# Performance work log

Hardware: AMD Instinct MI355X
Metric: run time of the kernel (lower is better)

Reference implementation:

```python
import jax, jax.numpy as jnp
import numpy as np

N_NODES = 100000
N_EDGES = 3200000
IN_CH, HID, OUT_CH = 11, 64, 1


def setup_inputs() -> dict:
    key = jax.random.key(0)
    ks = jax.random.split(key, 10)
    x = jax.random.normal(ks[0], (N_NODES, IN_CH), dtype=jnp.float32)
    edge_index = jax.random.randint(ks[1], (2, N_EDGES), 0, N_NODES, dtype=jnp.int64)
    s = lambda k, shape, fan_in: jax.random.normal(k, shape, jnp.float32) * (1.0 / np.sqrt(fan_in))
    return {
        "x": x,
        "edge_index": edge_index,
        # conv1: lin_l acts on aggregated neighbors (has bias), lin_r on root (no bias)
        "Wl1": s(ks[2], (HID, IN_CH), IN_CH), "bl1": jnp.zeros((HID,), jnp.float32),
        "Wr1": s(ks[3], (HID, IN_CH), IN_CH),
        "Wl2": s(ks[4], (HID, HID), HID), "bl2": jnp.zeros((HID,), jnp.float32),
        "Wr2": s(ks[5], (HID, HID), HID),
        "Wlin": s(ks[6], (OUT_CH, HID), HID), "blin": jnp.zeros((OUT_CH,), jnp.float32),
    }


def _sage_conv(x, src, dst, Wl, bl, Wr):
    # mean aggregation of source features onto destination nodes
    msg = x[src]                                            # [E, d] gather
    agg = jax.ops.segment_sum(msg, dst, num_segments=N_NODES)          # [N, d]
    cnt = jax.ops.segment_sum(jnp.ones_like(dst, jnp.float32), dst, num_segments=N_NODES)
    mean = agg / jnp.maximum(cnt, 1.0)[:, None]             # isolated nodes -> 0
    return mean @ Wl.T + bl + x @ Wr.T


def reference(x, edge_index, Wl1, bl1, Wr1, Wl2, bl2, Wr2, Wlin, blin):
    src, dst = edge_index[0], edge_index[1]
    h = jax.nn.relu(_sage_conv(x, src, dst, Wl1, bl1, Wr1))
    h = jax.nn.relu(_sage_conv(h, src, dst, Wl2, bl2, Wr2))
    return h @ Wlin.T + blin
```

## Files before the change

### kernel.cpp

```cpp
#include <hip/hip_runtime.h>
#include <hip/hip_fp16.h>

#define IN_CH 11
#define HID 64
#define PAD 64
#define OVCAP 16384
#define NBLK 1024
#define BSH 7

typedef _Float16 half8_t __attribute__((ext_vector_type(8)));
typedef float f32x4_t __attribute__((ext_vector_type(4)));

__global__ void k_prep(const float* __restrict__ x, const float* __restrict__ Wl2,
                       const float* __restrict__ Wr2, unsigned* __restrict__ xphu,
                       __half* __restrict__ wl2h, __half* __restrict__ wr2h,
                       int* __restrict__ ovcnt, int N) {
    int i = blockIdx.x * blockDim.x + threadIdx.x;
    if (i == 0) *ovcnt = 0;
    if (i < HID * HID) {
        wl2h[i] = __float2half_rn(Wl2[i]);
        wr2h[i] = __float2half_rn(Wr2[i]);
    }
    if (i < (N + 1) * 8) {
        int n = i >> 3, j = (i & 7) * 2;
        float a = 0.f, b = 0.f;
        if (n < N) {
            if (j < IN_CH) a = x[n * IN_CH + j];
            if (j + 1 < IN_CH) b = x[n * IN_CH + j + 1];
        }
        unsigned lo = (unsigned)__half_as_ushort(__float2half_rn(a));
        unsigned hi = (unsigned)__half_as_ushort(__float2half_rn(b));
        xphu[i] = lo | (hi << 16);
    }
}


__global__ __launch_bounds__(256) void k_hist(const int* __restrict__ dst,
        int* __restrict__ hist, int E, int csz, int nbkt) {
    __shared__ int h[800];
    int tid = threadIdx.x, blk = blockIdx.x;
    for (int t = tid; t < nbkt; t += 256) h[t] = 0;
    __syncthreads();
    int c0 = blk * csz, c1 = min(c0 + csz, E);
    for (int e = c0 + tid; e < c1; e += 256)
        atomicAdd(&h[dst[e] >> BSH], 1);
    __syncthreads();
    for (int t = tid; t < nbkt; t += 256) hist[t * NBLK + blk] = h[t];
}

__global__ __launch_bounds__(1024) void k_scanA(int* __restrict__ hist,
        int* __restrict__ btot) {
    __shared__ int wsum[16];
    int b = blockIdx.x, tid = threadIdx.x;
    int lane = tid & 63, wv = tid >> 6;
    int v = hist[b * NBLK + tid];
    int inc = v;
    #pragma unroll
    for (int off = 1; off < 64; off <<= 1) {
        int t = __shfl_up(inc, off);
        if (lane >= off) inc += t;
    }
    if (lane == 63) wsum[wv] = inc;
    __syncthreads();
    int base = 0;
    #pragma unroll
    for (int w = 0; w < 16; w++) base += (w < wv) ? wsum[w] : 0;
    hist[b * NBLK + tid] = base + inc - v;
    if (tid == NBLK - 1) btot[b] = base + inc;
}

__global__ __launch_bounds__(1024) void k_scanB(const int* __restrict__ btot,
        int* __restrict__ bstart, int nbkt) {
    __shared__ int wsum[16];
    int tid = threadIdx.x;
    int lane = tid & 63, wv = tid >> 6;
    int v = (tid < nbkt) ? btot[tid] : 0;
    int inc = v;
    #pragma unroll
    for (int off = 1; off < 64; off <<= 1) {
        int t = __shfl_up(inc, off);
        if (lane >= off) inc += t;
    }
    if (lane == 63) wsum[wv] = inc;
    __syncthreads();
    int base = 0;
    #pragma unroll
    for (int w = 0; w < 16; w++) base += (w < wv) ? wsum[w] : 0;
    if (tid < nbkt) bstart[tid] = base + inc - v;
}

__global__ __launch_bounds__(256) void k_scatter(const int* __restrict__ src,
        const int* __restrict__ dst, const int* __restrict__ hist,
        const int* __restrict__ bstart,
        unsigned* __restrict__ ebuf, int E, int csz, int nbkt) {
    __shared__ int cur[800];
    int tid = threadIdx.x, blk = blockIdx.x;
    for (int t = tid; t < nbkt; t += 256)
        cur[t] = hist[t * NBLK + blk] + bstart[t];
    __syncthreads();
    int c0 = blk * csz, c1 = min(c0 + csz, E);
    for (int e = c0 + tid; e < c1; e += 256) {
        int d = dst[e], s = src[e];
        int slot = atomicAdd(&cur[d >> BSH], 1);
        ebuf[slot] = ((unsigned)(d & 127) << 17) | (unsigned)s;
    }
}

__global__ __launch_bounds__(256) void k_bbuild(const unsigned* __restrict__ ebuf,
        const int* __restrict__ bstart, const int* __restrict__ btot,
        int* __restrict__ cnt, int* __restrict__ col64,
        int* __restrict__ ovcnt, int* __restrict__ ov, int N) {
    __shared__ int lc[128];
    __shared__ int colsh[128 * PAD];
    int tid = threadIdx.x, b = blockIdx.x;
    int lo = b << BSH, hi = min(lo + 128, N);
    #pragma unroll
    for (int i = 0; i < 8; i++)
        ((int4*)colsh)[tid + i * 256] = make_int4(N, N, N, N);
    if (tid < 128) lc[tid] = 0;
    __syncthreads();
    int cs = bstart[b], cc = btot[b];
    for (int i = tid; i < cc; i += 256) {
        unsigned v = ebuf[cs + i];
        int dl = (int)(v >> 17), s = (int)(v & 0x1FFFFu);
        int r = atomicAdd(&lc[dl], 1);
        if (r < PAD) {
            colsh[(dl << 6) | r] = s;
        } else {
            int q = atomicAdd(ovcnt, 1);
            if (q < OVCAP) { ov[2 * q] = lo + dl; ov[2 * q + 1] = s; }
        }
    }
    __syncthreads();
    int nn = hi - lo;
    int4* dst4 = (int4*)col64 + (size_t)lo * 16;
    for (int i = tid; i < nn * 16; i += 256) dst4[i] = ((int4*)colsh)[i];
    if (tid < nn) cnt[lo + tid] = lc[tid];
}

__global__ void k_agg1(const unsigned* __restrict__ xphu,
                       const int* __restrict__ col64,
                       float* __restrict__ agg1, int N) {
    int lane = threadIdx.x & 63;
    int n = blockIdx.x * 4 + (threadIdx.x >> 6);
    if (n >= N) return;
    int c8 = lane & 7, sub = lane >> 3;
    const int* cb = col64 + n * PAD;
    int s[8];
    #pragma unroll
    for (int jj = 0; jj < 8; jj++) s[jj] = cb[sub + 8 * jj];
    unsigned v[8];
    #pragma unroll
    for (int jj = 0; jj < 8; jj++) v[jj] = xphu[s[jj] * 8 + c8];
    __half2 a2 = __floats2half2_rn(0.f, 0.f);
    #pragma unroll
    for (int jj = 0; jj < 8; jj++) a2 = __hadd2(a2, *(__half2*)&v[jj]);
    float2 f = __half22float2(a2);
    #pragma unroll
    for (int off = 8; off <= 32; off <<= 1) {
        f.x += __shfl_xor(f.x, off);
        f.y += __shfl_xor(f.y, off);
    }
    if (lane < 8) ((float2*)agg1)[n * 8 + lane] = f;
}

__global__ void k_ov1(const int* __restrict__ ovcnt, const int* __restrict__ ov,
                      const float* __restrict__ x, float* __restrict__ agg1) {
    int c = *ovcnt; if (c > OVCAP) c = OVCAP;
    for (int i = blockIdx.x * blockDim.x + threadIdx.x; i < c;
         i += gridDim.x * blockDim.x) {
        int d = ov[2 * i], s = ov[2 * i + 1];
        for (int ch = 0; ch < IN_CH; ch++)
            atomicAdd(&agg1[d * 16 + ch], x[s * IN_CH + ch]);
    }
}

__global__ void k_dense1(const float* __restrict__ x, const float* __restrict__ agg1,
                         const int* __restrict__ cnt, const float* __restrict__ Wl,
                         const float* __restrict__ bl, const float* __restrict__ Wr,
                         unsigned* __restrict__ h1h, int N) {
    int lane = threadIdx.x & 63;
    int n = blockIdx.x * 4 + (threadIdx.x >> 6);
    if (n > N) return;
    if (n == N) {
        if (lane < 32) h1h[n * 32 + lane] = 0u;
        return;
    }
    int deg = cnt[n];
    float inv = deg > 0 ? 1.f / (float)deg : 0.f;
    float mv = (lane < 16) ? agg1[n * 16 + lane] * inv : 0.f;
    float xv = (lane < IN_CH) ? x[n * IN_CH + lane] : 0.f;
    float h = bl[lane];
    #pragma unroll
    for (int c = 0; c < IN_CH; c++)
        h += Wl[lane * IN_CH + c] * __shfl(mv, c) + Wr[lane * IN_CH + c] * __shfl(xv, c);
    h = fmaxf(h, 0.f);
    unsigned my = (unsigned)__half_as_ushort(__float2half_rn(h));
    unsigned nx = __shfl_down(my, 1);
    if ((lane & 1) == 0) h1h[n * 32 + (lane >> 1)] = my | (nx << 16);
}

__global__ void k_agg2(const uint4* __restrict__ h1h4, const int* __restrict__ col64,
                       float* __restrict__ agg2, int N) {
    int lane = threadIdx.x & 63;
    int n = blockIdx.x * 4 + (threadIdx.x >> 6);
    if (n >= N) return;
    int c8 = lane & 7, sub = lane >> 3;
    const int* cb = col64 + n * PAD;
    int s[8];
    #pragma unroll
    for (int jj = 0; jj < 8; jj++) s[jj] = cb[sub + 8 * jj];
    uint4 v[8];
    #pragma unroll
    for (int jj = 0; jj < 8; jj++) v[jj] = h1h4[s[jj] * 8 + c8];
    __half2 a2[4];
    #pragma unroll
    for (int t = 0; t < 4; t++) a2[t] = __floats2half2_rn(0.f, 0.f);
    #pragma unroll
    for (int jj = 0; jj < 8; jj++) {
        a2[0] = __hadd2(a2[0], *(__half2*)&v[jj].x);
        a2[1] = __hadd2(a2[1], *(__half2*)&v[jj].y);
        a2[2] = __hadd2(a2[2], *(__half2*)&v[jj].z);
        a2[3] = __hadd2(a2[3], *(__half2*)&v[jj].w);
    }
    float acc[8];
    #pragma unroll
    for (int t = 0; t < 4; t++) {
        float2 f = __half22float2(a2[t]);
        acc[2 * t] = f.x; acc[2 * t + 1] = f.y;
    }
    #pragma unroll
    for (int off = 8; off <= 32; off <<= 1) {
        #pragma unroll
        for (int t = 0; t < 8; t++) acc[t] += __shfl_xor(acc[t], off);
    }
    float val = acc[0];
    #pragma unroll
    for (int t = 1; t < 8; t++) if (sub == t) val = acc[t];
    agg2[n * 64 + 8 * c8 + sub] = val;
}

__global__ void k_ov2(const int* __restrict__ ovcnt, const int* __restrict__ ov,
                      const unsigned* __restrict__ h1h, float* __restrict__ agg2) {
    int c = *ovcnt; if (c > OVCAP) c = OVCAP;
    const __half* h1 = (const __half*)h1h;
    for (int i = blockIdx.x * blockDim.x + threadIdx.x; i < c;
         i += gridDim.x * blockDim.x) {
        int d = ov[2 * i], s = ov[2 * i + 1];
        for (int ch = 0; ch < HID; ch++)
            atomicAdd(&agg2[d * 64 + ch], __half2float(h1[s * 64 + ch]));
    }
}

__global__ __launch_bounds__(256) void k_dense2(
    const float4* __restrict__ agg2_4, const int* __restrict__ cnt,
    const uint4* __restrict__ h1h_u4,
    const __half* __restrict__ wl2h, const __half* __restrict__ wr2h,
    const float* __restrict__ bl, const float* __restrict__ Wlin,
    const float* __restrict__ blin, float* __restrict__ out, int N) {
    union U { uint4 u; half8_t h; };
    int lane = threadIdx.x & 63;
    int wave = blockIdx.x * 4 + (threadIdx.x >> 6);
    int nwaves = gridDim.x * 4;
    int r16 = lane & 15, quad = lane >> 4;
    const uint4* wlu = (const uint4*)wl2h;
    const uint4* wru = (const uint4*)wr2h;
    half8_t bfr[4][4];
    #pragma unroll
    for (int tt = 0; tt < 4; tt++) {
        int o = tt * 16 + r16;
        U t0, t1, t2, t3;
        t0.u = wlu[o * 8 + quad];
        t1.u = wlu[o * 8 + 4 + quad];
        t2.u = wru[o * 8 + quad];
        t3.u = wru[o * 8 + 4 + quad];
        bfr[tt][0] = t0.h; bfr[tt][1] = t1.h; bfr[tt][2] = t2.h; bfr[tt][3] = t3.h;
    }
    float bl_c[4], wl_c[4];
    #pragma unroll
    for (int tt = 0; tt < 4; tt++) {
        bl_c[tt] = bl[tt * 16 + r16];
        wl_c[tt] = Wlin[tt * 16 + r16];
    }
    float b0 = blin[0];
    int ntiles = (N + 15) >> 4;
    for (int t = wave; t < ntiles; t += nwaves) {
        int nb = t * 16;
        int n = nb + r16; if (n >= N) n = N - 1;
        int deg = cnt[n];
        float inv = deg > 0 ? 1.f / (float)deg : 0.f;
        float4 m0 = agg2_4[n * 16 + quad * 2];
        float4 m1 = agg2_4[n * 16 + quad * 2 + 1];
        float4 m2 = agg2_4[n * 16 + 8 + quad * 2];
        float4 m3 = agg2_4[n * 16 + 8 + quad * 2 + 1];
        half8_t a0h, a1h;
        a0h[0] = (_Float16)(m0.x * inv); a0h[1] = (_Float16)(m0.y * inv);
        a0h[2] = (_Float16)(m0.z * inv); a0h[3] = (_Float16)(m0.w * inv);
        a0h[4] = (_Float16)(m1.x * inv); a0h[5] = (_Float16)(m1.y * inv);
        a0h[6] = (_Float16)(m1.z * inv); a0h[7] = (_Float16)(m1.w * inv);
        a1h[0] = (_Float16)(m2.x * inv); a1h[1] = (_Float16)(m2.y * inv);
        a1h[2] = (_Float16)(m2.z * inv); a1h[3] = (_Float16)(m2.w * inv);
        a1h[4] = (_Float16)(m3.x * inv); a1h[5] = (_Float16)(m3.y * inv);
        a1h[6] = (_Float16)(m3.z * inv); a1h[7] = (_Float16)(m3.w * inv);
        U a2, a3;
        a2.u = h1h_u4[n * 8 + quad];
        a3.u = h1h_u4[n * 8 + 4 + quad];
        float p0 = 0.f, p1 = 0.f, p2 = 0.f, p3 = 0.f;
        #pragma unroll
        for (int tt = 0; tt < 4; tt++) {
            f32x4_t c = {0.f, 0.f, 0.f, 0.f};
            c = __builtin_amdgcn_mfma_f32_16x16x32_f16(a0h, bfr[tt][0], c, 0, 0, 0);
            c = __builtin_amdgcn_mfma_f32_16x16x32_f16(a1h, bfr[tt][1], c, 0, 0, 0);
            c = __builtin_amdgcn_mfma_f32_16x16x32_f16(a2.h, bfr[tt][2], c, 0, 0, 0);
            c = __builtin_amdgcn_mfma_f32_16x16x32_f16(a3.h, bfr[tt][3], c, 0, 0, 0);
            p0 += fmaxf(c[0] + bl_c[tt], 0.f) * wl_c[tt];
            p1 += fmaxf(c[1] + bl_c[tt], 0.f) * wl_c[tt];
            p2 += fmaxf(c[2] + bl_c[tt], 0.f) * wl_c[tt];
            p3 += fmaxf(c[3] + bl_c[tt], 0.f) * wl_c[tt];
        }
        #pragma unroll
        for (int off = 1; off <= 8; off <<= 1) {
            p0 += __shfl_xor(p0, off); p1 += __shfl_xor(p1, off);
            p2 += __shfl_xor(p2, off); p3 += __shfl_xor(p3, off);
        }
        if (r16 == 0) {
            int nn = nb + quad * 4;
            if (nn + 3 < N) {
                ((float4*)out)[nn >> 2] = make_float4(p0 + b0, p1 + b0, p2 + b0, p3 + b0);
            } else {
                if (nn + 0 < N) out[nn + 0] = p0 + b0;
                if (nn + 1 < N) out[nn + 1] = p1 + b0;
                if (nn + 2 < N) out[nn + 2] = p2 + b0;
                if (nn + 3 < N) out[nn + 3] = p3 + b0;
            }
        }
    }
}


extern "C" void kernel_launch(void* const* d_in, const int* in_sizes, int n_in,
                              void* d_out, int out_size, void* d_ws, size_t ws_size,
                              hipStream_t stream) {
    const float* x    = (const float*)d_in[0];
    const int*   ei   = (const int*)d_in[1];
    const float* Wl1  = (const float*)d_in[2];
    const float* bl1  = (const float*)d_in[3];
    const float* Wr1  = (const float*)d_in[4];
    const float* Wl2  = (const float*)d_in[5];
    const float* bl2  = (const float*)d_in[6];
    const float* Wr2  = (const float*)d_in[7];
    const float* Wlin = (const float*)d_in[8];
    const float* blin = (const float*)d_in[9];
    float* out = (float*)d_out;

    int N = in_sizes[0] / IN_CH;
    int E = in_sizes[1] / 2;
    const int* srcp = ei;
    const int* dstp = ei + E;

    int* ws       = (int*)d_ws;
    int* cnt      = ws;
    int* ovcnt    = ws + N;
    int* col64    = ws + 100032;
    int* hist     = ws + 100032;
    unsigned* xph = (unsigned*)(ws + 6500032);
    unsigned* ebuf = (unsigned*)(ws + 7300064);
    float* agg1   = (float*)(ws + 7300064);
    float* agg2   = (float*)(ws + 6500032);
    unsigned* h1h = (unsigned*)(ws + 12900096);
    int* ov       = ws + 16100128;
    __half* wl2h  = (__half*)(ws + 16132896);
    __half* wr2h  = (__half*)(ws + 16134944);
    int* btot     = ws + 16136992;
    int* bstart   = ws + 16138016;

    int nbkt = (N + 127) >> BSH;
    int csz  = (E + NBLK - 1) / NBLK;

    k_prep   <<<((N + 1) * 8 + 255) / 256, 256, 0, stream>>>(x, Wl2, Wr2, xph,
                                                             wl2h, wr2h, ovcnt, N);
    k_hist   <<<NBLK, 256, 0, stream>>>(dstp, hist, E, csz, nbkt);
    k_scanA  <<<nbkt, 1024, 0, stream>>>(hist, btot);
    k_scanB  <<<1, 1024, 0, stream>>>(btot, bstart, nbkt);
    k_scatter<<<NBLK, 256, 0, stream>>>(srcp, dstp, hist, bstart, ebuf, E, csz, nbkt);
    k_bbuild <<<nbkt, 256, 0, stream>>>(ebuf, bstart, btot, cnt, col64,
                                        ovcnt, ov, N);

    k_agg1   <<<(N + 3) / 4, 256, 0, stream>>>(xph, col64, agg1, N);
    k_ov1    <<<8, 256, 0, stream>>>(ovcnt, ov, x, agg1);
    k_dense1 <<<(N + 4) / 4, 256, 0, stream>>>(x, agg1, cnt, Wl1, bl1, Wr1, h1h, N);

    k_agg2   <<<(N + 3) / 4, 256, 0, stream>>>((const uint4*)h1h, col64, agg2, N);
    k_ov2    <<<8, 256, 0, stream>>>(ovcnt, ov, h1h, agg2);

    k_dense2 <<<512, 256, 0, stream>>>((const float4*)agg2, cnt, (const uint4*)h1h,
                                       wl2h, wr2h, bl2, Wlin, blin, out, N);
}
```

Measured before the change: 293.2 us.

## Coarsen edge bucketing to 1024-node buckets with 8 sub-block builds each

```diff
diff --git a/kernel.cpp b/kernel.cpp
--- a/kernel.cpp
+++ b/kernel.cpp
@@ -5,8 +5,8 @@
 #define HID 64
 #define PAD 64
 #define OVCAP 16384
-#define NBLK 1024
-#define BSH 7
+#define NBLK 512
+#define BSH 10
 
 typedef _Float16 half8_t __attribute__((ext_vector_type(8)));
 typedef float f32x4_t __attribute__((ext_vector_type(4)));
@@ -37,20 +37,20 @@
 
 __global__ __launch_bounds__(256) void k_hist(const int* __restrict__ dst,
         int* __restrict__ hist, int E, int csz, int nbkt) {
-    __shared__ int h[800];
+    __shared__ int h[128];
     int tid = threadIdx.x, blk = blockIdx.x;
-    for (int t = tid; t < nbkt; t += 256) h[t] = 0;
+    if (tid < 128) h[tid] = 0;
     __syncthreads();
     int c0 = blk * csz, c1 = min(c0 + csz, E);
     for (int e = c0 + tid; e < c1; e += 256)
         atomicAdd(&h[dst[e] >> BSH], 1);
     __syncthreads();
-    for (int t = tid; t < nbkt; t += 256) hist[t * NBLK + blk] = h[t];
-}
-
-__global__ __launch_bounds__(1024) void k_scanA(int* __restrict__ hist,
+    if (tid < nbkt) hist[tid * NBLK + blk] = h[tid];
+}
+
+__global__ __launch_bounds__(512) void k_scanA(int* __restrict__ hist,
         int* __restrict__ btot) {
-    __shared__ int wsum[16];
+    __shared__ int wsum[8];
     int b = blockIdx.x, tid = threadIdx.x;
     int lane = tid & 63, wv = tid >> 6;
     int v = hist[b * NBLK + tid];
@@ -64,14 +64,14 @@
     __syncthreads();
     int base = 0;
     #pragma unroll
-    for (int w = 0; w < 16; w++) base += (w < wv) ? wsum[w] : 0;
+    for (int w = 0; w < 8; w++) base += (w < wv) ? wsum[w] : 0;
     hist[b * NBLK + tid] = base + inc - v;
     if (tid == NBLK - 1) btot[b] = base + inc;
 }
 
-__global__ __launch_bounds__(1024) void k_scanB(const int* __restrict__ btot,
+__global__ __launch_bounds__(128) void k_scanB(const int* __restrict__ btot,
         int* __restrict__ bstart, int nbkt) {
-    __shared__ int wsum[16];
+    __shared__ int wsum[2];
     int tid = threadIdx.x;
     int lane = tid & 63, wv = tid >> 6;
     int v = (tid < nbkt) ? btot[tid] : 0;
@@ -83,9 +83,7 @@
     }
     if (lane == 63) wsum[wv] = inc;
     __syncthreads();
-    int base = 0;
-    #pragma unroll
-    for (int w = 0; w < 16; w++) base += (w < wv) ? wsum[w] : 0;
+    int base = (wv == 1) ? wsum[0] : 0;
     if (tid < nbkt) bstart[tid] = base + inc - v;
 }
 
@@ -93,16 +91,15 @@
         const int* __restrict__ dst, const int* __restrict__ hist,
         const int* __restrict__ bstart,
         unsigned* __restrict__ ebuf, int E, int csz, int nbkt) {
-    __shared__ int cur[800];
+    __shared__ int cur[128];
     int tid = threadIdx.x, blk = blockIdx.x;
-    for (int t = tid; t < nbkt; t += 256)
-        cur[t] = hist[t * NBLK + blk] + bstart[t];
+    if (tid < nbkt) cur[tid] = hist[tid * NBLK + blk] + bstart[tid];
     __syncthreads();
     int c0 = blk * csz, c1 = min(c0 + csz, E);
     for (int e = c0 + tid; e < c1; e += 256) {
         int d = dst[e], s = src[e];
         int slot = atomicAdd(&cur[d >> BSH], 1);
-        ebuf[slot] = ((unsigned)(d & 127) << 17) | (unsigned)s;
+        ebuf[slot] = ((unsigned)(d & 1023) << 17) | (unsigned)s;
     }
 }
 
@@ -112,8 +109,11 @@
         int* __restrict__ ovcnt, int* __restrict__ ov, int N) {
     __shared__ int lc[128];
     __shared__ int colsh[128 * PAD];
-    int tid = threadIdx.x, b = blockIdx.x;
-    int lo = b << BSH, hi = min(lo + 128, N);
+    int tid = threadIdx.x;
+    int b = blockIdx.x >> 3, sub = blockIdx.x & 7;
+    int lo = (b << BSH) + (sub << 7);
+    if (lo >= N) return;
+    int hi = min(lo + 128, N);
     #pragma unroll
     for (int i = 0; i < 8; i++)
         ((int4*)colsh)[tid + i * 256] = make_int4(N, N, N, N);
@@ -122,13 +122,16 @@
     int cs = bstart[b], cc = btot[b];
     for (int i = tid; i < cc; i += 256) {
         unsigned v = ebuf[cs + i];
-        int dl = (int)(v >> 17), s = (int)(v & 0x1FFFFu);
-        int r = atomicAdd(&lc[dl], 1);
-        if (r < PAD) {
-            colsh[(dl << 6) | r] = s;
-        } else {
-            int q = atomicAdd(ovcnt, 1);
-            if (q < OVCAP) { ov[2 * q] = lo + dl; ov[2 * q + 1] = s; }
+        int dl = (int)(v >> 17);
+        if ((dl >> 7) == sub) {
+            int s = (int)(v & 0x1FFFFu);
+            int r = atomicAdd(&lc[dl & 127], 1);
+            if (r < PAD) {
+                colsh[((dl & 127) << 6) | r] = s;
+            } else {
+                int q = atomicAdd(ovcnt, 1);
+                if (q < OVCAP) { ov[2 * q] = (b << BSH) + dl; ov[2 * q + 1] = s; }
+            }
         }
     }
     __syncthreads();
@@ -374,17 +377,17 @@
     int* btot     = ws + 16136992;
     int* bstart   = ws + 16138016;
 
-    int nbkt = (N + 127) >> BSH;
+    int nbkt = (N + 1023) >> BSH;
     int csz  = (E + NBLK - 1) / NBLK;
 
     k_prep   <<<((N + 1) * 8 + 255) / 256, 256, 0, stream>>>(x, Wl2, Wr2, xph,
                                                              wl2h, wr2h, ovcnt, N);
     k_hist   <<<NBLK, 256, 0, stream>>>(dstp, hist, E, csz, nbkt);
-    k_scanA  <<<nbkt, 1024, 0, stream>>>(hist, btot);
-    k_scanB  <<<1, 1024, 0, stream>>>(btot, bstart, nbkt);
+    k_scanA  <<<nbkt, NBLK, 0, stream>>>(hist, btot);
+    k_scanB  <<<1, 128, 0, stream>>>(btot, bstart, nbkt);
     k_scatter<<<NBLK, 256, 0, stream>>>(srcp, dstp, hist, bstart, ebuf, E, csz, nbkt);
-    k_bbuild <<<nbkt, 256, 0, stream>>>(ebuf, bstart, btot, cnt, col64,
-                                        ovcnt, ov, N);
+    k_bbuild <<<nbkt * 8, 256, 0, stream>>>(ebuf, bstart, btot, cnt, col64,
+                                            ovcnt, ov, N);
 
     k_agg1   <<<(N + 3) / 4, 256, 0, stream>>>(xph, col64, agg1, N);
     k_ov1    <<<8, 256, 0, stream>>>(ovcnt, ov, x, agg1);
```

After: 302.4 us. 1.03x slower.
